# Performance work log

Measured on AMD Instinct MI355X. Metric: run time of the kernel, lower is better.

Reference implementation:

```python
import jax
import jax.numpy as jnp
import numpy as np

N_NODES = 4096
N_EDGES = 65536
D_FEAT = 64


def setup_inputs() -> dict:
    key = jax.random.key(0)
    k1, k2, k3, k4 = jax.random.split(key, 4)
    x = jax.random.normal(k1, (N_NODES, D_FEAT), dtype=jnp.float32)
    edge_index = jax.random.randint(k2, (2, N_EDGES), 0, N_NODES, dtype=jnp.int32)
    batch = jnp.zeros((N_NODES,), dtype=jnp.int32)
    # GraphConv(in_channels, 1): lin_rel (with bias) on aggregated neighbors, lin_root on self
    w_rel = jax.random.normal(k3, (D_FEAT, 1), dtype=jnp.float32) * 0.1
    w_root = jax.random.normal(k4, (D_FEAT, 1), dtype=jnp.float32) * 0.1
    b = jnp.zeros((1,), dtype=jnp.float32)
    return {"x": x, "edge_index": edge_index, "batch": batch,
            "w_rel": w_rel, "w_root": w_root, "b": b}


def _merge_stars(x, src0, dst0, score):
    """Faithful sequential greedy star contraction (priority order by score desc)."""
    N = x.shape[0]
    order = jnp.argsort(-score)  # descending, ties like argsort

    def step(carry, node):
        xc, src, dst, remaining, center = carry
        active = remaining[node]
        # dests = set of targets of edges whose (current, rewritten) source == node,
        # minus already-chosen center nodes
        dest_edge = src == node                                  # [E]
        dest_node = jnp.zeros(N, bool).at[dst].max(dest_edge)    # node-level set
        dest_node = dest_node & ~center
        # torch does sum over list(dests)+[node]: node counted again (even on self-loop)
        combine = jnp.einsum('n,nd->d', dest_node.astype(xc.dtype), xc) + xc[node]
        D = dest_node.at[node].set(True)                         # dests U {node}
        x2 = xc.at[node].set(combine)
        src2 = jnp.where(D[src], node, src)                      # np.isin rewrite
        dst2 = jnp.where(D[dst], node, dst)
        rem2 = remaining & ~dest_node
        cen2 = center.at[node].set(True)
        carry2 = (jnp.where(active, x2, xc),
                  jnp.where(active, src2, src),
                  jnp.where(active, dst2, dst),
                  jnp.where(active, rem2, remaining),
                  jnp.where(active, cen2, center))
        return carry2, None

    init = (x, src0, dst0, jnp.ones(N, bool), jnp.zeros(N, bool))
    (x_final, _, _, remaining, _), _ = jax.lax.scan(step, init, order)
    return x_final, remaining


def reference(x, edge_index, batch, w_rel, w_root, b):
    N, d = x.shape
    src0, dst0 = edge_index[0], edge_index[1]
    # GraphConv score: W_rel * sum_{j->i} x_j + b + W_root * x_i ; dropout p=0; tanh
    agg = jax.ops.segment_sum(x[src0], dst0, num_segments=N)     # [N, d]
    score = jnp.tanh((agg @ w_rel + x @ w_root + b).reshape(-1)) # [N]

    x_final, remaining = _merge_stars(x, src0, dst0, score)

    # perm = sorted(nodes_remaining); outputs padded to static size N (sentinel -1)
    perm = jnp.nonzero(remaining, size=N, fill_value=N)[0]
    x_pooled = jnp.take(x_final, perm, axis=0, mode='fill', fill_value=0.0)
    kept = perm < N
    batch_pooled = jnp.where(kept, jnp.take(batch, jnp.minimum(perm, N - 1)), -1)
    # filter_adj on the ORIGINAL edge_index: keep edges with both endpoints kept,
    # relabel nodes to their rank among kept nodes; invalid edges -> -1
    relabel = jnp.cumsum(remaining.astype(jnp.int32)) - 1
    valid = remaining[src0] & remaining[dst0]
    new_src = jnp.where(valid, relabel[src0], -1)
    new_dst = jnp.where(valid, relabel[dst0], -1)
    new_edge_index = jnp.stack([new_src, new_dst])
    perm_out = jnp.where(kept, perm, -1)
    return x_pooled, new_edge_index, batch_pooled, perm_out
```

## Files before the change

### kernel.cpp

```cpp
#include <hip/hip_runtime.h>

#define NN 4096
#define NE 65536
#define ND 64

__global__ void k1_node_dots(const float* __restrict__ x, const float* __restrict__ wrel,
                             const float* __restrict__ wroot, double* __restrict__ srel,
                             double* __restrict__ sroot) {
    int gt = blockIdx.x * blockDim.x + threadIdx.x;
    int node = gt >> 6, lane = gt & 63;
    if (node >= NN) return;
    double xv = (double)x[node * ND + lane];
    double pr = xv * (double)wrel[lane];
    double po = xv * (double)wroot[lane];
    for (int off = 32; off > 0; off >>= 1) {
        pr += __shfl_down(pr, off);
        po += __shfl_down(po, off);
    }
    if (lane == 0) {
        srel[node] = pr;
        sroot[node] = po;
    }
}

__global__ void __launch_bounds__(1024) k34_contract(
        const double* __restrict__ srel, const double* __restrict__ sroot,
        const float* __restrict__ bptr, const int* __restrict__ ei,
        int* __restrict__ map_g, int* __restrict__ rem_g, int* __restrict__ relab_g,
        int* __restrict__ perm_a, int* __restrict__ nkeep_g) {
    __shared__ __align__(16) char buf[163840];
    unsigned short* incsr = (unsigned short*)buf;
    char* aux = buf + 131072;
    int* cursor = (int*)aux;
    double* srel_lds = (double*)aux;
    volatile unsigned long long* skey = (volatile unsigned long long*)aux;
    int* wt = (int*)(aux + 20544);
    int tid = threadIdx.x, lane = tid & 63, wv = tid >> 6;

    for (int n = tid; n < NN; n += 1024) cursor[n] = 0;
    __syncthreads();
    const int4* eid4 = (const int4*)(ei + NE);
    for (int i = tid; i < NE / 4; i += 1024) {
        int4 q = eid4[i];
        atomicAdd(&cursor[q.x], 1);
        atomicAdd(&cursor[q.y], 1);
        atomicAdd(&cursor[q.z], 1);
        atomicAdd(&cursor[q.w], 1);
    }
    __syncthreads();

    int t0 = cursor[4 * tid], t1 = cursor[4 * tid + 1];
    int t2 = cursor[4 * tid + 2], t3 = cursor[4 * tid + 3];
    int tot = t0 + t1 + t2 + t3;
    int inc = tot;
    for (int off = 1; off < 64; off <<= 1) {
        int v = __shfl_up(inc, off);
        if (lane >= off) inc += v;
    }
    if (lane == 63) wt[wv] = inc;
    __syncthreads();
    if (wv == 0 && lane < 16) {
        int v = wt[lane];
        for (int off = 1; off < 16; off <<= 1) {
            int u2 = __shfl_up(v, off);
            if (lane >= off) v += u2;
        }
        wt[lane] = v;
    }
    __syncthreads();
    int waveoff = (wv > 0) ? wt[wv - 1] : 0;
    int excl = waveoff + inc - tot;
    int rs4[4], re4[4];
    rs4[0] = excl; rs4[1] = excl + t0; rs4[2] = excl + t0 + t1; rs4[3] = excl + t0 + t1 + t2;
    cursor[4 * tid]     = rs4[0];
    cursor[4 * tid + 1] = rs4[1];
    cursor[4 * tid + 2] = rs4[2];
    cursor[4 * tid + 3] = rs4[3];
    __syncthreads();

    const int4* eis4 = (const int4*)ei;
    for (int i = tid; i < NE / 4; i += 1024) {
        int4 s = eis4[i];
        int4 d = eid4[i];
        incsr[atomicAdd(&cursor[d.x], 1)] = (unsigned short)s.x;
        incsr[atomicAdd(&cursor[d.y], 1)] = (unsigned short)s.y;
        incsr[atomicAdd(&cursor[d.z], 1)] = (unsigned short)s.z;
        incsr[atomicAdd(&cursor[d.w], 1)] = (unsigned short)s.w;
    }
    __syncthreads();
    for (int t = 0; t < 4; ++t) re4[t] = cursor[4 * tid + t];
    __syncthreads();

    {
        double2* sl2 = (double2*)aux;
        const double2* sg2 = (const double2*)srel;
        for (int i = tid; i < NN / 2; i += 1024) sl2[i] = sg2[i];
    }
    __syncthreads();

    double bv = (double)bptr[0];
    unsigned long long base4[4];
    for (int t = 0; t < 4; ++t) {
        int v = 4 * tid + t;
        double s = 0.0;
        for (int e = rs4[t]; e < re4[t]; ++e) s += srel_lds[(int)incsr[e]];
        double arg = s + sroot[v] + bv;
        float sc = tanhf((float)arg);
        unsigned m = __float_as_uint(sc);
        m = (m & 0x80000000u) ? ~m : (m | 0x80000000u);
        base4[t] = ((unsigned long long)(~m) << 14) | ((unsigned long long)v << 2);
    }
    __syncthreads();

    for (int t = 0; t < 4; ++t) skey[4 * tid + t] = base4[t];
    __syncthreads();

    unsigned long long pk4[4], minC4[4];
    unsigned resolved = 0, centerm = 0, selfm = 0;
    for (int t = 0; t < 4; ++t) {
        int v = 4 * tid + t;
        unsigned long long pkv = base4[t] >> 2;
        pk4[t] = pkv;
        minC4[t] = ~0ULL;
        int w = rs4[t];
        for (int e = rs4[t]; e < re4[t]; ++e) {
            int u = (int)incsr[e];
            if (u == v) { selfm |= 1u << t; continue; }
            unsigned long long ku = skey[u] >> 2;
            if (ku < pkv) incsr[w++] = (unsigned short)u;
        }
        re4[t] = w;
        if (w == rs4[t]) {
            map_g[v] = v;
            skey[v] = base4[t] | 1ULL;
            centerm |= 1u << t; resolved |= 1u << t;
        }
    }

    int guard = 0;
    while (resolved != 0xFu && guard < 1000000) {
        ++guard;
        bool prog = false;
        for (int t = 0; t < 4; ++t) {
            if (resolved & (1u << t)) continue;
            int v = 4 * tid + t;
            int lo = rs4[t], hi = re4[t];
            unsigned long long minU = ~0ULL, mC = minC4[t];
            int w = lo;
            for (int e = lo; e < hi; ++e) {
                int u = (int)incsr[e];
                unsigned long long sk = skey[u];
                int st = (int)(sk & 3ULL);
                unsigned long long ku = sk >> 2;
                if (st == 0) { incsr[w++] = (unsigned short)u; if (ku < minU) minU = ku; }
                else if (st == 1) { if (ku < mC) mC = ku; }
            }
            if (w != hi) prog = true;
            re4[t] = w; minC4[t] = mC;
            if (mC < minU) {
                map_g[v] = (int)((mC >> 2) & 0xFFFULL);
                skey[v] = (pk4[t] << 2) | 2ULL;
                resolved |= 1u << t; prog = true;
            } else if (w == lo) {
                map_g[v] = v;
                skey[v] = (pk4[t] << 2) | 1ULL;
                centerm |= 1u << t; resolved |= 1u << t; prog = true;
            }
        }
        if (!prog) __builtin_amdgcn_s_sleep(1);
    }
    __syncthreads();

    int remb[4], cnt4 = 0;
    for (int t = 0; t < 4; ++t) {
        remb[t] = ((centerm >> t) & 1) && !((selfm >> t) & 1);
        cnt4 += remb[t];
    }
    int inc2 = cnt4;
    for (int off = 1; off < 64; off <<= 1) {
        int v = __shfl_up(inc2, off);
        if (lane >= off) inc2 += v;
    }
    if (lane == 63) wt[wv] = inc2;
    __syncthreads();
    if (wv == 0 && lane < 16) {
        int v = wt[lane];
        for (int off = 1; off < 16; off <<= 1) {
            int u2 = __shfl_up(v, off);
            if (lane >= off) v += u2;
        }
        wt[lane] = v;
    }
    __syncthreads();
    int woff2 = (wv > 0) ? wt[wv - 1] : 0;
    int run = woff2 + inc2 - cnt4;
    for (int t = 0; t < 4; ++t) {
        int v = 4 * tid + t;
        relab_g[v] = run;
        if (remb[t]) { perm_a[run] = v; ++run; }
        rem_g[v] = remb[t];
    }
    if (tid == 1023) nkeep_g[0] = run;
}

__global__ void k56_outputs(const float* __restrict__ x, const int* __restrict__ map_g,
                            const int* __restrict__ rem_g, const int* __restrict__ relab_g,
                            const int* __restrict__ perm_a, const int* __restrict__ ei,
                            const int* __restrict__ batch, const int* __restrict__ nkeep_g,
                            float* __restrict__ out) {
    int idx = blockIdx.x * blockDim.x + threadIdx.x;
    if (idx < NN * ND) {
        int n = idx >> 6, d = idx & 63;
        int m = map_g[n];
        if (rem_g[m]) atomicAdd(&out[relab_g[m] * ND + d], x[idx]);
    } else if (idx < NN * ND + 2 * NE) {
        int e = idx - NN * ND;
        int row = e >> 16;
        int ee = e & (NE - 1);
        int s = ei[ee], t = ei[NE + ee];
        bool valid = (rem_g[s] != 0) && (rem_g[t] != 0);
        int endp = (row == 0) ? s : t;
        out[idx] = valid ? (float)relab_g[endp] : -1.0f;
    } else if (idx < NN * ND + 2 * NE + NN) {
        int r = idx - (NN * ND + 2 * NE);
        int nk = nkeep_g[0];
        out[idx] = (r < nk) ? (float)batch[perm_a[r]] : -1.0f;
    } else if (idx < NN * ND + 2 * NE + 2 * NN) {
        int r = idx - (NN * ND + 2 * NE + NN);
        int nk = nkeep_g[0];
        out[idx] = (r < nk) ? (float)perm_a[r] : -1.0f;
    }
}

extern "C" void kernel_launch(void* const* d_in, const int* in_sizes, int n_in,
                              void* d_out, int out_size, void* d_ws, size_t ws_size,
                              hipStream_t stream) {
    const float* x     = (const float*)d_in[0];
    const int*   ei    = (const int*)d_in[1];
    const int*   batch = (const int*)d_in[2];
    const float* wrel  = (const float*)d_in[3];
    const float* wroot = (const float*)d_in[4];
    const float* b     = (const float*)d_in[5];

    char* ws = (char*)d_ws;
    double* srel  = (double*)(ws + 0);
    double* sroot = (double*)(ws + 32768);
    int*    map_g = (int*)(ws + 65536);
    int*    rem_g = (int*)(ws + 81920);
    int*    relab = (int*)(ws + 98304);
    int*    perma = (int*)(ws + 114688);
    int*    nkeep = (int*)(ws + 131072);

    float* out = (float*)d_out;

    hipMemsetAsync(out, 0, NN * ND * sizeof(float), stream);
    k1_node_dots<<<NN * ND / 256, 256, 0, stream>>>(x, wrel, wroot, srel, sroot);
    k34_contract<<<1, 1024, 0, stream>>>(srel, sroot, b, ei, map_g, rem_g, relab,
                                         perma, nkeep);
    int total_out = NN * ND + 2 * NE + 2 * NN;
    k56_outputs<<<(total_out + 255) / 256, 256, 0, stream>>>(x, map_g, rem_g, relab,
                                                             perma, ei, batch, nkeep, out);
}
```

Measured before the change: 160.7 us.

## Track min unresolved neighbor to skip full rescans; fuse output memset into k1

```diff
diff --git a/kernel.cpp b/kernel.cpp
--- a/kernel.cpp
+++ b/kernel.cpp
@@ -6,10 +6,10 @@
 
 __global__ void k1_node_dots(const float* __restrict__ x, const float* __restrict__ wrel,
                              const float* __restrict__ wroot, double* __restrict__ srel,
-                             double* __restrict__ sroot) {
+                             double* __restrict__ sroot, float* __restrict__ out) {
     int gt = blockIdx.x * blockDim.x + threadIdx.x;
+    out[gt] = 0.0f;
     int node = gt >> 6, lane = gt & 63;
-    if (node >= NN) return;
     double xv = (double)x[node * ND + lane];
     double pr = xv * (double)wrel[lane];
     double po = xv * (double)wroot[lane];
@@ -115,59 +115,77 @@
     for (int t = 0; t < 4; ++t) skey[4 * tid + t] = base4[t];
     __syncthreads();
 
-    unsigned long long pk4[4], minC4[4];
+    unsigned long long pk4[4], minC4[4], kMin4[4];
+    int uMin4[4];
     unsigned resolved = 0, centerm = 0, selfm = 0;
+
+#define DECIDE(t, v)                                                            \
+    if (minC4[t] < kMin4[t]) {                                                  \
+        map_g[v] = (int)(minC4[t] & 0xFFFULL);                                  \
+        skey[v] = (pk4[t] << 2) | 2ULL;                                         \
+        resolved |= 1u << t;                                                    \
+    } else if (kMin4[t] == ~0ULL) {                                             \
+        map_g[v] = v;                                                           \
+        skey[v] = (pk4[t] << 2) | 1ULL;                                         \
+        centerm |= 1u << t; resolved |= 1u << t;                                \
+    }
+
+#define RESCAN(t, v) {                                                          \
+        int lo = rs4[t], hi = re4[t], w = lo;                                   \
+        unsigned long long minU = ~0ULL; int um = -1;                           \
+        unsigned long long mc = minC4[t];                                       \
+        for (int e = lo; e < hi; ++e) {                                         \
+            int u = (int)incsr[e];                                              \
+            unsigned long long sk = skey[u];                                    \
+            int st = (int)(sk & 3ULL);                                          \
+            unsigned long long kq = sk >> 2;                                    \
+            if (st == 0) { incsr[w++] = (unsigned short)u;                      \
+                           if (kq < minU) { minU = kq; um = u; } }              \
+            else if (st == 1) { if (kq < mc) mc = kq; }                         \
+        }                                                                       \
+        re4[t] = w; minC4[t] = mc; kMin4[t] = minU; uMin4[t] = um;              \
+        DECIDE(t, v)                                                            \
+    }
+
     for (int t = 0; t < 4; ++t) {
         int v = 4 * tid + t;
         unsigned long long pkv = base4[t] >> 2;
         pk4[t] = pkv;
         minC4[t] = ~0ULL;
+        unsigned long long minU = ~0ULL; int um = -1;
+        unsigned long long mc = ~0ULL;
         int w = rs4[t];
         for (int e = rs4[t]; e < re4[t]; ++e) {
             int u = (int)incsr[e];
             if (u == v) { selfm |= 1u << t; continue; }
-            unsigned long long ku = skey[u] >> 2;
-            if (ku < pkv) incsr[w++] = (unsigned short)u;
-        }
-        re4[t] = w;
-        if (w == rs4[t]) {
-            map_g[v] = v;
-            skey[v] = base4[t] | 1ULL;
-            centerm |= 1u << t; resolved |= 1u << t;
-        }
+            unsigned long long sk = skey[u];
+            unsigned long long kq = sk >> 2;
+            if (kq >= pkv) continue;
+            int st = (int)(sk & 3ULL);
+            if (st == 0) { incsr[w++] = (unsigned short)u;
+                           if (kq < minU) { minU = kq; um = u; } }
+            else if (st == 1) { if (kq < mc) mc = kq; }
+        }
+        re4[t] = w; minC4[t] = mc; kMin4[t] = minU; uMin4[t] = um;
+        DECIDE(t, v)
     }
 
     int guard = 0;
-    while (resolved != 0xFu && guard < 1000000) {
+    while (resolved != 0xFu && guard < 2000000) {
         ++guard;
-        bool prog = false;
         for (int t = 0; t < 4; ++t) {
             if (resolved & (1u << t)) continue;
             int v = 4 * tid + t;
-            int lo = rs4[t], hi = re4[t];
-            unsigned long long minU = ~0ULL, mC = minC4[t];
-            int w = lo;
-            for (int e = lo; e < hi; ++e) {
-                int u = (int)incsr[e];
-                unsigned long long sk = skey[u];
-                int st = (int)(sk & 3ULL);
-                unsigned long long ku = sk >> 2;
-                if (st == 0) { incsr[w++] = (unsigned short)u; if (ku < minU) minU = ku; }
-                else if (st == 1) { if (ku < mC) mC = ku; }
+            unsigned long long sk = skey[uMin4[t]];
+            int st = (int)(sk & 3ULL);
+            if (st == 1) {
+                map_g[v] = uMin4[t];
+                skey[v] = (pk4[t] << 2) | 2ULL;
+                resolved |= 1u << t;
+            } else if (st == 2) {
+                RESCAN(t, v)
             }
-            if (w != hi) prog = true;
-            re4[t] = w; minC4[t] = mC;
-            if (mC < minU) {
-                map_g[v] = (int)((mC >> 2) & 0xFFFULL);
-                skey[v] = (pk4[t] << 2) | 2ULL;
-                resolved |= 1u << t; prog = true;
-            } else if (w == lo) {
-                map_g[v] = v;
-                skey[v] = (pk4[t] << 2) | 1ULL;
-                centerm |= 1u << t; resolved |= 1u << t; prog = true;
-            }
-        }
-        if (!prog) __builtin_amdgcn_s_sleep(1);
+        }
     }
     __syncthreads();
 
@@ -201,6 +219,8 @@
         rem_g[v] = remb[t];
     }
     if (tid == 1023) nkeep_g[0] = run;
+#undef RESCAN
+#undef DECIDE
 }
 
 __global__ void k56_outputs(const float* __restrict__ x, const int* __restrict__ map_g,
@@ -253,8 +273,7 @@
 
     float* out = (float*)d_out;
 
-    hipMemsetAsync(out, 0, NN * ND * sizeof(float), stream);
-    k1_node_dots<<<NN * ND / 256, 256, 0, stream>>>(x, wrel, wroot, srel, sroot);
+    k1_node_dots<<<NN * ND / 256, 256, 0, stream>>>(x, wrel, wroot, srel, sroot, out);
     k34_contract<<<1, 1024, 0, stream>>>(srel, sroot, b, ei, map_g, rem_g, relab,
                                          perma, nkeep);
     int total_out = NN * ND + 2 * NE + 2 * NN;
```

After: 171.9 us. +7.0%, slower.

## Fuse pipeline into one cooperative kernel with grid-parallel bucketed CSR build

Applied to the files above, without the earlier changes.

```diff
diff --git a/kernel.cpp b/kernel.cpp
--- a/kernel.cpp
+++ b/kernel.cpp
@@ -1,234 +1,234 @@
 #include <hip/hip_runtime.h>
+#include <hip/hip_cooperative_groups.h>
+
+namespace cg = cooperative_groups;
 
 #define NN 4096
 #define NE 65536
 #define ND 64
-
-__global__ void k1_node_dots(const float* __restrict__ x, const float* __restrict__ wrel,
-                             const float* __restrict__ wroot, double* __restrict__ srel,
-                             double* __restrict__ sroot) {
-    int gt = blockIdx.x * blockDim.x + threadIdx.x;
-    int node = gt >> 6, lane = gt & 63;
-    if (node >= NN) return;
-    double xv = (double)x[node * ND + lane];
-    double pr = xv * (double)wrel[lane];
-    double po = xv * (double)wroot[lane];
-    for (int off = 32; off > 0; off >>= 1) {
-        pr += __shfl_down(pr, off);
-        po += __shfl_down(po, off);
-    }
-    if (lane == 0) {
-        srel[node] = pr;
-        sroot[node] = po;
-    }
-}
-
-__global__ void __launch_bounds__(1024) k34_contract(
-        const double* __restrict__ srel, const double* __restrict__ sroot,
-        const float* __restrict__ bptr, const int* __restrict__ ei,
+#define BCAP 44
+#define NBLK 128
+#define NTHR 1024
+
+__global__ void __launch_bounds__(1024) mega(
+        const float* __restrict__ x, const int* __restrict__ ei,
+        const int* __restrict__ batch, const float* __restrict__ wrel,
+        const float* __restrict__ wroot, const float* __restrict__ bptr,
+        double* __restrict__ srel, double* __restrict__ sroot,
         int* __restrict__ map_g, int* __restrict__ rem_g, int* __restrict__ relab_g,
-        int* __restrict__ perm_a, int* __restrict__ nkeep_g) {
+        int* __restrict__ perm_a, int* __restrict__ nkeep_g,
+        int* __restrict__ gcnt, unsigned short* __restrict__ gbuf,
+        float* __restrict__ out) {
+    cg::grid_group grid = cg::this_grid();
     __shared__ __align__(16) char buf[163840];
-    unsigned short* incsr = (unsigned short*)buf;
-    char* aux = buf + 131072;
-    int* cursor = (int*)aux;
-    double* srel_lds = (double*)aux;
-    volatile unsigned long long* skey = (volatile unsigned long long*)aux;
-    int* wt = (int*)(aux + 20544);
     int tid = threadIdx.x, lane = tid & 63, wv = tid >> 6;
-
-    for (int n = tid; n < NN; n += 1024) cursor[n] = 0;
-    __syncthreads();
-    const int4* eid4 = (const int4*)(ei + NE);
-    for (int i = tid; i < NE / 4; i += 1024) {
-        int4 q = eid4[i];
-        atomicAdd(&cursor[q.x], 1);
-        atomicAdd(&cursor[q.y], 1);
-        atomicAdd(&cursor[q.z], 1);
-        atomicAdd(&cursor[q.w], 1);
-    }
-    __syncthreads();
-
-    int t0 = cursor[4 * tid], t1 = cursor[4 * tid + 1];
-    int t2 = cursor[4 * tid + 2], t3 = cursor[4 * tid + 3];
-    int tot = t0 + t1 + t2 + t3;
-    int inc = tot;
-    for (int off = 1; off < 64; off <<= 1) {
-        int v = __shfl_up(inc, off);
-        if (lane >= off) inc += v;
-    }
-    if (lane == 63) wt[wv] = inc;
-    __syncthreads();
-    if (wv == 0 && lane < 16) {
-        int v = wt[lane];
-        for (int off = 1; off < 16; off <<= 1) {
-            int u2 = __shfl_up(v, off);
-            if (lane >= off) v += u2;
-        }
-        wt[lane] = v;
-    }
-    __syncthreads();
-    int waveoff = (wv > 0) ? wt[wv - 1] : 0;
-    int excl = waveoff + inc - tot;
-    int rs4[4], re4[4];
-    rs4[0] = excl; rs4[1] = excl + t0; rs4[2] = excl + t0 + t1; rs4[3] = excl + t0 + t1 + t2;
-    cursor[4 * tid]     = rs4[0];
-    cursor[4 * tid + 1] = rs4[1];
-    cursor[4 * tid + 2] = rs4[2];
-    cursor[4 * tid + 3] = rs4[3];
-    __syncthreads();
-
-    const int4* eis4 = (const int4*)ei;
-    for (int i = tid; i < NE / 4; i += 1024) {
-        int4 s = eis4[i];
-        int4 d = eid4[i];
-        incsr[atomicAdd(&cursor[d.x], 1)] = (unsigned short)s.x;
-        incsr[atomicAdd(&cursor[d.y], 1)] = (unsigned short)s.y;
-        incsr[atomicAdd(&cursor[d.z], 1)] = (unsigned short)s.z;
-        incsr[atomicAdd(&cursor[d.w], 1)] = (unsigned short)s.w;
-    }
-    __syncthreads();
-    for (int t = 0; t < 4; ++t) re4[t] = cursor[4 * tid + t];
-    __syncthreads();
-
-    {
-        double2* sl2 = (double2*)aux;
-        const double2* sg2 = (const double2*)srel;
-        for (int i = tid; i < NN / 2; i += 1024) sl2[i] = sg2[i];
-    }
-    __syncthreads();
-
-    double bv = (double)bptr[0];
-    unsigned long long base4[4];
-    for (int t = 0; t < 4; ++t) {
-        int v = 4 * tid + t;
-        double s = 0.0;
-        for (int e = rs4[t]; e < re4[t]; ++e) s += srel_lds[(int)incsr[e]];
-        double arg = s + sroot[v] + bv;
-        float sc = tanhf((float)arg);
-        unsigned m = __float_as_uint(sc);
-        m = (m & 0x80000000u) ? ~m : (m | 0x80000000u);
-        base4[t] = ((unsigned long long)(~m) << 14) | ((unsigned long long)v << 2);
-    }
-    __syncthreads();
-
-    for (int t = 0; t < 4; ++t) skey[4 * tid + t] = base4[t];
-    __syncthreads();
-
-    unsigned long long pk4[4], minC4[4];
-    unsigned resolved = 0, centerm = 0, selfm = 0;
-    for (int t = 0; t < 4; ++t) {
-        int v = 4 * tid + t;
-        unsigned long long pkv = base4[t] >> 2;
-        pk4[t] = pkv;
-        minC4[t] = ~0ULL;
-        int w = rs4[t];
-        for (int e = rs4[t]; e < re4[t]; ++e) {
-            int u = (int)incsr[e];
-            if (u == v) { selfm |= 1u << t; continue; }
-            unsigned long long ku = skey[u] >> 2;
-            if (ku < pkv) incsr[w++] = (unsigned short)u;
-        }
-        re4[t] = w;
-        if (w == rs4[t]) {
-            map_g[v] = v;
-            skey[v] = base4[t] | 1ULL;
-            centerm |= 1u << t; resolved |= 1u << t;
-        }
-    }
-
-    int guard = 0;
-    while (resolved != 0xFu && guard < 1000000) {
-        ++guard;
-        bool prog = false;
-        for (int t = 0; t < 4; ++t) {
-            if (resolved & (1u << t)) continue;
-            int v = 4 * tid + t;
-            int lo = rs4[t], hi = re4[t];
-            unsigned long long minU = ~0ULL, mC = minC4[t];
-            int w = lo;
-            for (int e = lo; e < hi; ++e) {
+    int gtid = blockIdx.x * NTHR + tid;
+    int gstride = NBLK * NTHR;
+
+    int gwave = gtid >> 6;
+    for (int node = gwave; node < NN; node += (gstride >> 6)) {
+        double xv = (double)x[node * ND + lane];
+        double pr = xv * (double)wrel[lane];
+        double po = xv * (double)wroot[lane];
+        for (int off = 32; off > 0; off >>= 1) {
+            pr += __shfl_down(pr, off);
+            po += __shfl_down(po, off);
+        }
+        if (lane == 0) { srel[node] = pr; sroot[node] = po; }
+    }
+    for (int e = gtid; e < NE; e += gstride) {
+        int s = ei[e], d = ei[NE + e];
+        int pos = atomicAdd(&gcnt[d], 1);
+        if (pos < BCAP) gbuf[d * BCAP + pos] = (unsigned short)s;
+    }
+    __threadfence();
+    grid.sync();
+
+    if (blockIdx.x == 0) {
+        unsigned short* incsr = (unsigned short*)buf;
+        char* aux = buf + 131072;
+        double* srel_lds = (double*)aux;
+        volatile unsigned long long* skey = (volatile unsigned long long*)aux;
+        int* wt = (int*)(aux + 20544);
+
+        int4 d4 = ((const int4*)gcnt)[tid];
+        int t0 = min(d4.x, BCAP), t1 = min(d4.y, BCAP);
+        int t2 = min(d4.z, BCAP), t3 = min(d4.w, BCAP);
+        int tot = t0 + t1 + t2 + t3;
+        int inc = tot;
+        for (int off = 1; off < 64; off <<= 1) {
+            int v = __shfl_up(inc, off);
+            if (lane >= off) inc += v;
+        }
+        if (lane == 63) wt[wv] = inc;
+        __syncthreads();
+        if (wv == 0 && lane < 16) {
+            int v = wt[lane];
+            for (int off = 1; off < 16; off <<= 1) {
+                int u2 = __shfl_up(v, off);
+                if (lane >= off) v += u2;
+            }
+            wt[lane] = v;
+        }
+        __syncthreads();
+        int waveoff = (wv > 0) ? wt[wv - 1] : 0;
+        int excl = waveoff + inc - tot;
+        int rs4[4], re4[4];
+        rs4[0] = excl; rs4[1] = excl + t0; rs4[2] = excl + t0 + t1;
+        rs4[3] = excl + t0 + t1 + t2;
+        re4[0] = rs4[1]; re4[1] = rs4[2]; re4[2] = rs4[3]; re4[3] = rs4[3] + t3;
+        __syncthreads();
+
+        for (int t = 0; t < 4; ++t) {
+            int v = 4 * tid + t;
+            const unsigned short* gp = gbuf + v * BCAP;
+            int base = rs4[t], dg = re4[t] - rs4[t];
+            int j = 0;
+            for (; j + 4 <= dg; j += 4) {
+                ushort4 q = *(const ushort4*)(gp + j);
+                incsr[base + j] = q.x; incsr[base + j + 1] = q.y;
+                incsr[base + j + 2] = q.z; incsr[base + j + 3] = q.w;
+            }
+            for (; j < dg; ++j) incsr[base + j] = gp[j];
+        }
+
+        {
+            double2* sl2 = (double2*)aux;
+            const double2* sg2 = (const double2*)srel;
+            for (int i = tid; i < NN / 2; i += 1024) sl2[i] = sg2[i];
+        }
+        __syncthreads();
+
+        double bv = (double)bptr[0];
+        unsigned long long base4[4];
+        for (int t = 0; t < 4; ++t) {
+            int v = 4 * tid + t;
+            double s = 0.0;
+            for (int e = rs4[t]; e < re4[t]; ++e) s += srel_lds[(int)incsr[e]];
+            double arg = s + sroot[v] + bv;
+            float sc = tanhf((float)arg);
+            unsigned m = __float_as_uint(sc);
+            m = (m & 0x80000000u) ? ~m : (m | 0x80000000u);
+            base4[t] = ((unsigned long long)(~m) << 14) | ((unsigned long long)v << 2);
+        }
+        __syncthreads();
+
+        for (int t = 0; t < 4; ++t) skey[4 * tid + t] = base4[t];
+        __syncthreads();
+
+        unsigned long long pk4[4], minC4[4];
+        unsigned resolved = 0, centerm = 0, selfm = 0;
+        for (int t = 0; t < 4; ++t) {
+            int v = 4 * tid + t;
+            unsigned long long pkv = base4[t] >> 2;
+            pk4[t] = pkv; minC4[t] = ~0ULL;
+            int w = rs4[t];
+            for (int e = rs4[t]; e < re4[t]; ++e) {
                 int u = (int)incsr[e];
-                unsigned long long sk = skey[u];
-                int st = (int)(sk & 3ULL);
-                unsigned long long ku = sk >> 2;
-                if (st == 0) { incsr[w++] = (unsigned short)u; if (ku < minU) minU = ku; }
-                else if (st == 1) { if (ku < mC) mC = ku; }
-            }
-            if (w != hi) prog = true;
-            re4[t] = w; minC4[t] = mC;
-            if (mC < minU) {
-                map_g[v] = (int)((mC >> 2) & 0xFFFULL);
-                skey[v] = (pk4[t] << 2) | 2ULL;
-                resolved |= 1u << t; prog = true;
-            } else if (w == lo) {
+                if (u == v) { selfm |= 1u << t; continue; }
+                unsigned long long ku = skey[u] >> 2;
+                if (ku < pkv) incsr[w++] = (unsigned short)u;
+            }
+            re4[t] = w;
+            if (w == rs4[t]) {
                 map_g[v] = v;
-                skey[v] = (pk4[t] << 2) | 1ULL;
-                centerm |= 1u << t; resolved |= 1u << t; prog = true;
-            }
-        }
-        if (!prog) __builtin_amdgcn_s_sleep(1);
-    }
-    __syncthreads();
-
-    int remb[4], cnt4 = 0;
-    for (int t = 0; t < 4; ++t) {
-        remb[t] = ((centerm >> t) & 1) && !((selfm >> t) & 1);
-        cnt4 += remb[t];
-    }
-    int inc2 = cnt4;
-    for (int off = 1; off < 64; off <<= 1) {
-        int v = __shfl_up(inc2, off);
-        if (lane >= off) inc2 += v;
-    }
-    if (lane == 63) wt[wv] = inc2;
-    __syncthreads();
-    if (wv == 0 && lane < 16) {
-        int v = wt[lane];
-        for (int off = 1; off < 16; off <<= 1) {
-            int u2 = __shfl_up(v, off);
-            if (lane >= off) v += u2;
-        }
-        wt[lane] = v;
-    }
-    __syncthreads();
-    int woff2 = (wv > 0) ? wt[wv - 1] : 0;
-    int run = woff2 + inc2 - cnt4;
-    for (int t = 0; t < 4; ++t) {
-        int v = 4 * tid + t;
-        relab_g[v] = run;
-        if (remb[t]) { perm_a[run] = v; ++run; }
-        rem_g[v] = remb[t];
-    }
-    if (tid == 1023) nkeep_g[0] = run;
-}
-
-__global__ void k56_outputs(const float* __restrict__ x, const int* __restrict__ map_g,
-                            const int* __restrict__ rem_g, const int* __restrict__ relab_g,
-                            const int* __restrict__ perm_a, const int* __restrict__ ei,
-                            const int* __restrict__ batch, const int* __restrict__ nkeep_g,
-                            float* __restrict__ out) {
-    int idx = blockIdx.x * blockDim.x + threadIdx.x;
-    if (idx < NN * ND) {
-        int n = idx >> 6, d = idx & 63;
-        int m = map_g[n];
-        if (rem_g[m]) atomicAdd(&out[relab_g[m] * ND + d], x[idx]);
-    } else if (idx < NN * ND + 2 * NE) {
-        int e = idx - NN * ND;
-        int row = e >> 16;
-        int ee = e & (NE - 1);
-        int s = ei[ee], t = ei[NE + ee];
-        bool valid = (rem_g[s] != 0) && (rem_g[t] != 0);
-        int endp = (row == 0) ? s : t;
-        out[idx] = valid ? (float)relab_g[endp] : -1.0f;
-    } else if (idx < NN * ND + 2 * NE + NN) {
-        int r = idx - (NN * ND + 2 * NE);
-        int nk = nkeep_g[0];
-        out[idx] = (r < nk) ? (float)batch[perm_a[r]] : -1.0f;
-    } else if (idx < NN * ND + 2 * NE + 2 * NN) {
-        int r = idx - (NN * ND + 2 * NE + NN);
-        int nk = nkeep_g[0];
-        out[idx] = (r < nk) ? (float)perm_a[r] : -1.0f;
+                skey[v] = base4[t] | 1ULL;
+                centerm |= 1u << t; resolved |= 1u << t;
+            }
+        }
+
+        int guard = 0;
+        while (resolved != 0xFu && guard < 1000000) {
+            ++guard;
+            bool prog = false;
+            for (int t = 0; t < 4; ++t) {
+                if (resolved & (1u << t)) continue;
+                int v = 4 * tid + t;
+                int lo = rs4[t], hi = re4[t];
+                unsigned long long minU = ~0ULL, mC = minC4[t];
+                int w = lo;
+                for (int e = lo; e < hi; ++e) {
+                    int u = (int)incsr[e];
+                    unsigned long long sk = skey[u];
+                    int st = (int)(sk & 3ULL);
+                    unsigned long long ku = sk >> 2;
+                    if (st == 0) { incsr[w++] = (unsigned short)u;
+                                   if (ku < minU) minU = ku; }
+                    else if (st == 1) { if (ku < mC) mC = ku; }
+                }
+                if (w != hi) prog = true;
+                re4[t] = w; minC4[t] = mC;
+                if (mC < minU) {
+                    map_g[v] = (int)(mC & 0xFFFULL);
+                    skey[v] = (pk4[t] << 2) | 2ULL;
+                    resolved |= 1u << t; prog = true;
+                } else if (w == lo) {
+                    map_g[v] = v;
+                    skey[v] = (pk4[t] << 2) | 1ULL;
+                    centerm |= 1u << t; resolved |= 1u << t; prog = true;
+                }
+            }
+            if (!prog) __builtin_amdgcn_s_sleep(1);
+        }
+        __syncthreads();
+
+        int remb[4], cnt4 = 0;
+        for (int t = 0; t < 4; ++t) {
+            remb[t] = ((centerm >> t) & 1) && !((selfm >> t) & 1);
+            cnt4 += remb[t];
+        }
+        int inc2 = cnt4;
+        for (int off = 1; off < 64; off <<= 1) {
+            int v = __shfl_up(inc2, off);
+            if (lane >= off) inc2 += v;
+        }
+        if (lane == 63) wt[wv] = inc2;
+        __syncthreads();
+        if (wv == 0 && lane < 16) {
+            int v = wt[lane];
+            for (int off = 1; off < 16; off <<= 1) {
+                int u2 = __shfl_up(v, off);
+                if (lane >= off) v += u2;
+            }
+            wt[lane] = v;
+        }
+        __syncthreads();
+        int woff2 = (wv > 0) ? wt[wv - 1] : 0;
+        int run = woff2 + inc2 - cnt4;
+        for (int t = 0; t < 4; ++t) {
+            int v = 4 * tid + t;
+            relab_g[v] = run;
+            if (remb[t]) { perm_a[run] = v; ++run; }
+            rem_g[v] = remb[t];
+        }
+        if (tid == 1023) nkeep_g[0] = run;
+    }
+    __threadfence();
+    grid.sync();
+
+    int total = NN * ND + 2 * NE + 2 * NN;
+    for (int idx = gtid; idx < total; idx += gstride) {
+        if (idx < NN * ND) {
+            int n = idx >> 6, d = idx & 63;
+            int m = map_g[n];
+            if (rem_g[m]) atomicAdd(&out[relab_g[m] * ND + d], x[idx]);
+        } else if (idx < NN * ND + 2 * NE) {
+            int e = idx - NN * ND;
+            int row = e >> 16;
+            int ee = e & (NE - 1);
+            int s = ei[ee], t = ei[NE + ee];
+            bool valid = (rem_g[s] != 0) && (rem_g[t] != 0);
+            int endp = (row == 0) ? s : t;
+            out[idx] = valid ? (float)relab_g[endp] : -1.0f;
+        } else if (idx < NN * ND + 2 * NE + NN) {
+            int r = idx - (NN * ND + 2 * NE);
+            int nk = nkeep_g[0];
+            out[idx] = (r < nk) ? (float)batch[perm_a[r]] : -1.0f;
+        } else {
+            int r = idx - (NN * ND + 2 * NE + NN);
+            int nk = nkeep_g[0];
+            out[idx] = (r < nk) ? (float)perm_a[r] : -1.0f;
+        }
     }
 }
 
@@ -243,21 +243,24 @@
     const float* b     = (const float*)d_in[5];
 
     char* ws = (char*)d_ws;
-    double* srel  = (double*)(ws + 0);
-    double* sroot = (double*)(ws + 32768);
-    int*    map_g = (int*)(ws + 65536);
-    int*    rem_g = (int*)(ws + 81920);
-    int*    relab = (int*)(ws + 98304);
-    int*    perma = (int*)(ws + 114688);
-    int*    nkeep = (int*)(ws + 131072);
+    double*         srel  = (double*)(ws + 0);
+    double*         sroot = (double*)(ws + 32768);
+    int*            map_g = (int*)(ws + 65536);
+    int*            rem_g = (int*)(ws + 81920);
+    int*            relab = (int*)(ws + 98304);
+    int*            perma = (int*)(ws + 114688);
+    int*            nkeep = (int*)(ws + 131072);
+    int*            gcnt  = (int*)(ws + 131200);
+    unsigned short* gbuf  = (unsigned short*)(ws + 147584);
 
     float* out = (float*)d_out;
 
+    hipMemsetAsync(gcnt, 0, NN * sizeof(int), stream);
     hipMemsetAsync(out, 0, NN * ND * sizeof(float), stream);
-    k1_node_dots<<<NN * ND / 256, 256, 0, stream>>>(x, wrel, wroot, srel, sroot);
-    k34_contract<<<1, 1024, 0, stream>>>(srel, sroot, b, ei, map_g, rem_g, relab,
-                                         perma, nkeep);
-    int total_out = NN * ND + 2 * NE + 2 * NN;
-    k56_outputs<<<(total_out + 255) / 256, 256, 0, stream>>>(x, map_g, rem_g, relab,
-                                                             perma, ei, batch, nkeep, out);
+
+    void* args[] = { (void*)&x, (void*)&ei, (void*)&batch, (void*)&wrel, (void*)&wroot,
+                     (void*)&b, (void*)&srel, (void*)&sroot, (void*)&map_g, (void*)&rem_g,
+                     (void*)&relab, (void*)&perma, (void*)&nkeep, (void*)&gcnt,
+                     (void*)&gbuf, (void*)&out };
+    hipLaunchCooperativeKernel((void*)mega, dim3(NBLK), dim3(NTHR), args, 0, stream);
 }
```

Measured after the change: 305.9 us. 1.9x slower.
